# Performance work log

Hardware: AMD Instinct MI355X
Metric: run time of the kernel (lower is better)

## Reference

```python
import jax, jax.numpy as jnp
import numpy as np

T, D = 4096, 2048
H, DK, DV = 6, 256, 512        # heads, head_k_dim, head_v_dim (expand_v=2)
KD, VD = H * DK, H * DV        # 1536, 3072
KSZ = 4                        # conv_size
GEN = D // 8                   # generator reduction 8 -> 256
EPS = 1e-5                     # norm_eps


def setup_inputs() -> dict:
    key = jax.random.key(0)
    ks = jax.random.split(key, 12)
    std = 0.02
    p = lambda i, shape: jax.random.normal(ks[i], shape, jnp.float32) * std
    rng = np.random.default_rng(0)
    A = rng.uniform(0.0, 16.0, H).astype(np.float32)
    dt = np.exp(rng.uniform(0, 1, H) * (np.log(0.1) - np.log(0.001)) + np.log(0.001)).astype(np.float32)
    dt = np.clip(dt, 1e-4, None)
    inv_dt = (dt + np.log(-np.expm1(-dt))).astype(np.float32)
    return {
        'hidden_states': jax.random.normal(ks[0], (T, D), jnp.float32),
        'Wq': p(1, (D, KD)), 'Wk': p(2, (D, KD)), 'Wv': p(3, (D, VD)),
        'Wb': p(4, (D, H)), 'Wa': p(5, (D, H)), 'Wg': p(6, (D, VD)), 'Wo': p(7, (VD, D)),
        'A_log': jnp.asarray(np.log(A)), 'dt_bias': jnp.asarray(inv_dt),
        'conv_w': p(8, (VD, KSZ)), 'gen_w1': p(9, (D, GEN)), 'gen_w2': p(10, (GEN, KSZ)),
        'norm_w': jnp.ones((DV,), jnp.float32),
    }


def _l2norm(x):
    return x * jax.lax.rsqrt(jnp.sum(x * x, -1, keepdims=True) + 1e-6)


def reference(hidden_states, Wq, Wk, Wv, Wb, Wa, Wg, Wo, A_log, dt_bias, conv_w, gen_w1, gen_w2, norm_w):
    h = hidden_states[None]                             # [1,T,D]
    q = jax.nn.silu(h @ Wq)                             # [1,T,KD]
    k = jax.nn.silu(h @ Wk)
    x = h @ Wv                                          # [1,T,VD]
    # dynamic short convolution: per-token kernel added to static depthwise kernel
    dyn = jax.nn.silu(h @ gen_w1) @ gen_w2              # [1,T,KSZ]
    xpad = jnp.pad(x, ((0, 0), (KSZ - 1, 0), (0, 0)))   # causal padding
    v = jnp.zeros_like(x)
    for j in range(KSZ):
        v = v + (conv_w[None, None, :, j] + dyn[:, :, None, j]) * xpad[:, j:j + x.shape[1], :]
    v = jax.nn.silu(v)

    B = 1
    q = _l2norm(q.reshape(B, -1, H, DK))                # use_qk_l2norm_in_kernel=True
    k = _l2norm(k.reshape(B, -1, H, DK))
    v = v.reshape(B, -1, H, DV)
    beta = jax.nn.sigmoid(h @ Wb)                       # [1,T,H]
    g = -jnp.exp(A_log) * jax.nn.softplus(h @ Wa + dt_bias)  # [1,T,H] decay log-gates
    scale = DK ** -0.5

    def step(S, inp):                                   # gated delta rule recurrence
        qt, kt, vt, gt, bt = inp
        S = S * jnp.exp(gt)[..., None, None]            # [B,H,DK,DV]
        dv = (vt - jnp.einsum('bhk,bhkv->bhv', kt, S)) * bt[..., None]
        S = S + kt[..., :, None] * dv[..., None, :]
        ot = jnp.einsum('bhk,bhkv->bhv', qt, S) * scale
        return S, ot

    S0 = jnp.zeros((B, H, DK, DV), jnp.float32)
    tm = lambda a: jnp.moveaxis(a, 1, 0)                # time-major for scan
    _, o = jax.lax.scan(step, S0, (tm(q), tm(k), tm(v), tm(g), tm(beta)))
    o = jnp.moveaxis(o, 0, 1)                           # [1,T,H,DV]

    gate = (h @ Wg).reshape(B, -1, H, DV)
    rms = jax.lax.rsqrt(jnp.mean(o * o, -1, keepdims=True) + EPS)
    o = o * rms * norm_w * jax.nn.silu(gate)            # gated RMSNorm
    o = o.reshape(B, -1, VD) @ Wo                       # [1,T,D]
    return o[0]
```

## Files before the change

### kernel.cpp

```cpp
#include <hip/hip_runtime.h>
#include <hip/hip_bf16.h>
#include <math.h>

#define T_LEN 4096
#define DIM   2048
#define NH    6
#define DK    256
#define DVh   512
#define KD    1536
#define VD    3072
#define CK    64
#define NCHK  (T_LEN / CK)

typedef __attribute__((ext_vector_type(8))) short bf16x8;
typedef __attribute__((ext_vector_type(4))) float f32x4;

__device__ __forceinline__ float silu_f(float v){ return v / (1.f + __expf(-v)); }

__device__ __forceinline__ unsigned short f2bf(float f) {
  unsigned int u = __float_as_uint(f);
  unsigned int r = u + 0x7FFFu + ((u >> 16) & 1u);
  return (unsigned short)(r >> 16);
}
__device__ __forceinline__ float bf2f(unsigned short s) {
  return __uint_as_float(((unsigned int)s) << 16);
}

__global__ __launch_bounds__(256) void cast_bf16(
    const float* __restrict__ in, unsigned short* __restrict__ out)
{
  int i = blockIdx.x * 256 + threadIdx.x;
  float4 v4 = ((const float4*)in)[i];
  ushort4 o4;
  o4.x = f2bf(v4.x); o4.y = f2bf(v4.y); o4.z = f2bf(v4.z); o4.w = f2bf(v4.w);
  ((ushort4*)out)[i] = o4;
}

__global__ __launch_bounds__(256) void tcast(
    const float* __restrict__ in, unsigned short* __restrict__ out, int R, int Cn)
{
  __shared__ float tile[32][33];
  int bx = blockIdx.x * 32;
  int by = blockIdx.y * 32;
  int tx = threadIdx.x & 31, ty = threadIdx.x >> 5;
#pragma unroll
  for (int i = 0; i < 32; i += 8)
    tile[ty + i][tx] = in[(size_t)(by + ty + i) * Cn + bx + tx];
  __syncthreads();
#pragma unroll
  for (int i = 0; i < 32; i += 8)
    out[(size_t)(bx + ty + i) * R + by + tx] = f2bf(tile[tx][ty + i]);
}

__global__ __launch_bounds__(256) void gemm_bt_bf16(
    const unsigned short* __restrict__ A, const unsigned short* __restrict__ BT,
    void* __restrict__ Cout, int M, int N, int K, int act)
{
  __shared__ unsigned short As[128 * 32];
  __shared__ unsigned short Bs[128 * 32];
  const int tid = threadIdx.x;
  const int bm = blockIdx.y * 128, bn = blockIdx.x * 128;
  const int lane = tid & 63, wave = tid >> 6;
  const int wm = (wave >> 1) * 64, wn = (wave & 1) * 64;
  const int fr = lane & 15, kq = lane >> 4;

  f32x4 acc[4][4];
#pragma unroll
  for (int i = 0; i < 4; ++i)
#pragma unroll
    for (int j = 0; j < 4; ++j) acc[i][j] = (f32x4){0.f, 0.f, 0.f, 0.f};

  const int r0 = tid >> 2, c0 = (tid & 3) * 8;
  const int r1 = r0 + 64;

  for (int k0 = 0; k0 < K; k0 += 32) {
    __builtin_amdgcn_global_load_lds(
        (const __attribute__((address_space(1))) unsigned int*)(A + (size_t)(bm + r0) * K + k0 + c0),
        (__attribute__((address_space(3))) unsigned int*)(As + r0 * 32 + c0), 16, 0, 0);
    __builtin_amdgcn_global_load_lds(
        (const __attribute__((address_space(1))) unsigned int*)(A + (size_t)(bm + r1) * K + k0 + c0),
        (__attribute__((address_space(3))) unsigned int*)(As + r1 * 32 + c0), 16, 0, 0);
    __builtin_amdgcn_global_load_lds(
        (const __attribute__((address_space(1))) unsigned int*)(BT + (size_t)(bn + r0) * K + k0 + c0),
        (__attribute__((address_space(3))) unsigned int*)(Bs + r0 * 32 + c0), 16, 0, 0);
    __builtin_amdgcn_global_load_lds(
        (const __attribute__((address_space(1))) unsigned int*)(BT + (size_t)(bn + r1) * K + k0 + c0),
        (__attribute__((address_space(3))) unsigned int*)(Bs + r1 * 32 + c0), 16, 0, 0);
    __syncthreads();

    bf16x8 af[4], bfr[4];
#pragma unroll
    for (int i = 0; i < 4; ++i)
      af[i] = *(const bf16x8*)(As + (wm + i * 16 + fr) * 32 + kq * 8);
#pragma unroll
    for (int j = 0; j < 4; ++j)
      bfr[j] = *(const bf16x8*)(Bs + (wn + j * 16 + fr) * 32 + kq * 8);
#pragma unroll
    for (int i = 0; i < 4; ++i)
#pragma unroll
      for (int j = 0; j < 4; ++j)
        acc[i][j] = __builtin_amdgcn_mfma_f32_16x16x32_bf16(af[i], bfr[j], acc[i][j], 0, 0, 0);
    __syncthreads();
  }

  if (act == 2) {
    unsigned short* C = (unsigned short*)Cout;
#pragma unroll
    for (int i = 0; i < 4; ++i) {
      int rbase = bm + wm + i * 16 + kq * 4;
#pragma unroll
      for (int r = 0; r < 4; ++r) {
        size_t rowoff = (size_t)(rbase + r) * N + bn + wn + fr;
#pragma unroll
        for (int j = 0; j < 4; ++j) C[rowoff + j * 16] = f2bf(acc[i][j][r]);
      }
    }
  } else {
    float* C = (float*)Cout;
#pragma unroll
    for (int i = 0; i < 4; ++i) {
      int rbase = bm + wm + i * 16 + kq * 4;
#pragma unroll
      for (int r = 0; r < 4; ++r) {
        size_t rowoff = (size_t)(rbase + r) * N + bn + wn + fr;
#pragma unroll
        for (int j = 0; j < 4; ++j) {
          float v = acc[i][j][r];
          if (act == 1) v = silu_f(v);
          C[rowoff + j * 16] = v;
        }
      }
    }
  }
}

__global__ __launch_bounds__(256) void proj_dyn(
    const float* __restrict__ tg, const float* __restrict__ w2, float* __restrict__ dyn)
{
  int t = blockIdx.x, tid = threadIdx.x;
  float g = tg[(size_t)t * 256 + tid];
  float p[4];
#pragma unroll
  for (int j = 0; j < 4; ++j) p[j] = g * w2[tid * 4 + j];
#pragma unroll
  for (int j = 0; j < 4; ++j)
    for (int m = 32; m >= 1; m >>= 1) p[j] += __shfl_xor(p[j], m);
  __shared__ float red[4][4];
  if ((tid & 63) == 0) {
    int w = tid >> 6;
#pragma unroll
    for (int j = 0; j < 4; ++j) red[w][j] = p[j];
  }
  __syncthreads();
  if (tid < 4) dyn[(size_t)t * 4 + tid] = red[0][tid] + red[1][tid] + red[2][tid] + red[3][tid];
}

__global__ __launch_bounds__(256) void proj_bg(
    const float* __restrict__ h, const float* __restrict__ Wb, const float* __restrict__ Wa,
    const float* __restrict__ A_log, const float* __restrict__ dt_bias,
    float* __restrict__ beta, float* __restrict__ gout)
{
  int t = blockIdx.x, tid = threadIdx.x;
  float pb[6], pa[6];
#pragma unroll
  for (int j = 0; j < 6; ++j) { pb[j] = 0.f; pa[j] = 0.f; }
  for (int d = tid; d < DIM; d += 256) {
    float hv = h[(size_t)t * DIM + d];
#pragma unroll
    for (int j = 0; j < 6; ++j) {
      pb[j] += hv * Wb[d * 6 + j];
      pa[j] += hv * Wa[d * 6 + j];
    }
  }
#pragma unroll
  for (int j = 0; j < 6; ++j)
    for (int m = 32; m >= 1; m >>= 1) { pb[j] += __shfl_xor(pb[j], m); pa[j] += __shfl_xor(pa[j], m); }
  __shared__ float rb[4][6], ra[4][6];
  if ((tid & 63) == 0) {
    int w = tid >> 6;
#pragma unroll
    for (int j = 0; j < 6; ++j) { rb[w][j] = pb[j]; ra[w][j] = pa[j]; }
  }
  __syncthreads();
  if (tid < 6) {
    int j = tid;
    float sb = rb[0][j] + rb[1][j] + rb[2][j] + rb[3][j];
    float sa = ra[0][j] + ra[1][j] + ra[2][j] + ra[3][j];
    beta[(size_t)t * 6 + j] = 1.f / (1.f + expf(-sb));
    float z = sa + dt_bias[j];
    float sp = (z > 20.f) ? z : log1pf(expf(z));
    gout[(size_t)t * 6 + j] = -expf(A_log[j]) * sp;
  }
}

__global__ __launch_bounds__(256) void conv_kernel(
    const float* __restrict__ x, const float* __restrict__ dyn,
    const float* __restrict__ cw, float* __restrict__ v)
{
  int c = blockIdx.x * 256 + threadIdx.x;
  int t = blockIdx.y;
  float4 w4 = ((const float4*)cw)[c];
  float d0 = dyn[t * 4 + 0], d1 = dyn[t * 4 + 1], d2 = dyn[t * 4 + 2], d3 = dyn[t * 4 + 3];
  float acc = (w4.w + d3) * x[(size_t)t * VD + c];
  if (t >= 1) acc += (w4.z + d2) * x[(size_t)(t - 1) * VD + c];
  if (t >= 2) acc += (w4.y + d1) * x[(size_t)(t - 2) * VD + c];
  if (t >= 3) acc += (w4.x + d0) * x[(size_t)(t - 3) * VD + c];
  v[(size_t)t * VD + c] = silu_f(acc);
}

__global__ __launch_bounds__(64) void l2norm_qk(
    float* __restrict__ q, float* __restrict__ k)
{
  size_t base = (size_t)blockIdx.x * 256;
  int tid = threadIdx.x;
  float4 qv = ((float4*)(q + base))[tid];
  float4 kv = ((float4*)(k + base))[tid];
  float sq = qv.x*qv.x + qv.y*qv.y + qv.z*qv.z + qv.w*qv.w;
  float sk = kv.x*kv.x + kv.y*kv.y + kv.z*kv.z + kv.w*kv.w;
  for (int m = 32; m >= 1; m >>= 1) { sq += __shfl_xor(sq, m); sk += __shfl_xor(sk, m); }
  float rq = rsqrtf(sq + 1e-6f) * 0.0625f;
  float rk = rsqrtf(sk + 1e-6f);
  qv.x *= rq; qv.y *= rq; qv.z *= rq; qv.w *= rq;
  kv.x *= rk; kv.y *= rk; kv.z *= rk; kv.w *= rk;
  ((float4*)(q + base))[tid] = qv;
  ((float4*)(k + base))[tid] = kv;
}

__global__ __launch_bounds__(64) void cumsum_g(
    const float* __restrict__ g, float* __restrict__ c, float* __restrict__ gammas)
{
  int ch = blockIdx.x, h = blockIdx.y;
  int t0 = ch * CK;
  int lane = threadIdx.x;
  float cum = g[(size_t)(t0 + lane) * 6 + h];
  for (int off = 1; off < 64; off <<= 1) {
    float n = __shfl_up(cum, off);
    if (lane >= off) cum += n;
  }
  c[(size_t)h * T_LEN + t0 + lane] = cum;
  if (lane == 63) gammas[h * NCHK + ch] = __expf(cum);
}

__global__ __launch_bounds__(384) void scale_kq(
    const float* __restrict__ q, const float* __restrict__ k, const float* __restrict__ c,
    unsigned short* __restrict__ Qb, unsigned short* __restrict__ Kb)
{
  int t = blockIdx.x;
  int tid = threadIdx.x;
  int h = tid >> 6;
  float w1 = __expf(c[(size_t)h * T_LEN + t]);
  size_t off = (size_t)t * KD + tid * 4;
  float4 qv = *(const float4*)(q + off);
  float4 kv = *(const float4*)(k + off);
  ushort4 qo, ko;
  qo.x = f2bf(w1 * qv.x); qo.y = f2bf(w1 * qv.y); qo.z = f2bf(w1 * qv.z); qo.w = f2bf(w1 * qv.w);
  ko.x = f2bf(w1 * kv.x); ko.y = f2bf(w1 * kv.y); ko.z = f2bf(w1 * kv.z); ko.w = f2bf(w1 * kv.w);
  *(ushort4*)(Qb + off) = qo;
  *(ushort4*)(Kb + off) = ko;
}

__global__ __launch_bounds__(256) void make_khT(
    const float* __restrict__ k, const float* __restrict__ c,
    unsigned short* __restrict__ KhT)
{
  int ch = blockIdx.x, h = blockIdx.y;
  int t0 = ch * CK;
  int tt = threadIdx.x & 63, ks = threadIdx.x >> 6;
  float cend = c[(size_t)h * T_LEN + t0 + 63];
  float w2 = __expf(cend - c[(size_t)h * T_LEN + t0 + tt]);
  size_t obase = ((size_t)(h * NCHK + ch)) * DK * CK;
#pragma unroll 8
  for (int kb2 = 0; kb2 < 64; ++kb2) {
    int kk = ks * 64 + kb2;
    float kv = k[(size_t)(t0 + tt) * KD + h * 256 + kk];
    KhT[obase + (size_t)kk * CK + tt] = f2bf(w2 * kv);
  }
}

__global__ __launch_bounds__(256) void chunk_lp(
    const float* __restrict__ q, const float* __restrict__ k,
    const float* __restrict__ c, const float* __restrict__ beta,
    float* __restrict__ Lg, unsigned short* __restrict__ Pm)
{
  const int ch = blockIdx.x, h = blockIdx.y;
  const int t0 = ch * CK;
  const int tid = threadIdx.x;
  const int w = tid >> 6, lane = tid & 63, fr = lane & 15, kq = lane >> 4;
  __shared__ unsigned short kb[64][264];
  __shared__ unsigned short qb[64][264];
  __shared__ float cs[64], bs[64];
#pragma unroll
  for (int i = 0; i < 16; ++i) {
    int fi = tid + i * 256;
    int r = fi >> 6, d4 = fi & 63;
    float4 kv = *(const float4*)(k + (size_t)(t0 + r) * KD + h * 256 + d4 * 4);
    float4 qv = *(const float4*)(q + (size_t)(t0 + r) * KD + h * 256 + d4 * 4);
    ushort4 k4, q4;
    k4.x = f2bf(kv.x); k4.y = f2bf(kv.y); k4.z = f2bf(kv.z); k4.w = f2bf(kv.w);
    q4.x = f2bf(qv.x); q4.y = f2bf(qv.y); q4.z = f2bf(qv.z); q4.w = f2bf(qv.w);
    *(ushort4*)&kb[r][d4 * 4] = k4;
    *(ushort4*)&qb[r][d4 * 4] = q4;
  }
  if (tid < 64) {
    cs[tid] = c[(size_t)h * T_LEN + t0 + tid];
    bs[tid] = beta[(size_t)(t0 + tid) * 6 + h];
  }
  __syncthreads();

  f32x4 akk[4], aqk[4];
#pragma unroll
  for (int j = 0; j < 4; ++j) { akk[j] = (f32x4){0,0,0,0}; aqk[j] = (f32x4){0,0,0,0}; }
#pragma unroll
  for (int kt = 0; kt < 8; ++kt) {
    bf16x8 ak = *(const bf16x8*)&kb[16 * w + fr][kt * 32 + kq * 8];
    bf16x8 aq = *(const bf16x8*)&qb[16 * w + fr][kt * 32 + kq * 8];
#pragma unroll
    for (int j = 0; j < 4; ++j) {
      bf16x8 b = *(const bf16x8*)&kb[j * 16 + fr][kt * 32 + kq * 8];
      akk[j] = __builtin_amdgcn_mfma_f32_16x16x32_bf16(ak, b, akk[j], 0, 0, 0);
      aqk[j] = __builtin_amdgcn_mfma_f32_16x16x32_bf16(aq, b, aqk[j], 0, 0, 0);
    }
  }
  size_t base = ((size_t)(h * NCHK + ch)) * CK * CK;
#pragma unroll
  for (int j = 0; j < 4; ++j) {
#pragma unroll
    for (int r = 0; r < 4; ++r) {
      int t = 16 * w + kq * 4 + r, col = j * 16 + fr;
      float e = __expf(fminf(cs[t] - cs[col], 0.f));
      Lg[base + t * 64 + col] = (col < t) ? bs[t] * e * akk[j][r] : 0.f;
      Pm[base + t * 64 + col] = f2bf((col <= t) ? e * aqk[j][r] : 0.f);
    }
  }
}

__global__ __launch_bounds__(64) void tri_inv(
    const float* __restrict__ Lg, const float* __restrict__ beta,
    unsigned short* __restrict__ Tm)
{
  const int ch = blockIdx.x, h = blockIdx.y;
  const size_t base = ((size_t)(h * NCHK + ch)) * CK * CK;
  const int j = threadIdx.x;
  __shared__ float Ll[64][65];
  __shared__ float Tl[64][65];
  for (int t = 0; t < 64; ++t) Ll[t][j] = Lg[base + t * 64 + j];
  __syncthreads();
  for (int t = 0; t < 64; ++t) {
    float s;
    if (j > t) s = 0.f;
    else if (j == t) s = 1.f;
    else {
      s = 0.f;
      for (int m = j; m < t; ++m) s -= Ll[t][m] * Tl[m][j];
    }
    Tl[t][j] = s;
  }
  float bj = beta[(size_t)(ch * 64 + j) * 6 + h];
  for (int t = 0; t < 64; ++t) Tm[base + t * 64 + j] = f2bf(Tl[t][j] * bj);
}

__global__ __launch_bounds__(256) void scan_chunk(
    const unsigned short* __restrict__ Kb,
    const unsigned short* __restrict__ Qb,
    const unsigned short* __restrict__ KhT,
    const unsigned short* __restrict__ Tm,
    const unsigned short* __restrict__ Pm,
    const float* __restrict__ gammas,
    float* __restrict__ VO)
{
  const int h = blockIdx.y, sl = blockIdx.x;
  const int tid = threadIdx.x;
  const int w = tid >> 6, lane = tid & 63;
  const int fr = lane & 15, kq = lane >> 4;

  __shared__ unsigned short S0h[16][264];
  __shared__ unsigned short S0l[16][264];
  __shared__ unsigned short XT[16][72];
  __shared__ unsigned short DVT[16][72];

  f32x4 st[4];
#pragma unroll
  for (int i = 0; i < 4; ++i) st[i] = (f32x4){0.f, 0.f, 0.f, 0.f};

  const int colg = h * DVh + sl * 16 + fr;
  const size_t hc0 = (size_t)h * NCHK;

  for (int ch = 0; ch < NCHK; ++ch) {
    const int t0 = ch * CK;
    const size_t cb = hc0 + ch;

    bf16x8 kf[8], qf[8];
    {
      const unsigned short* krow = Kb + (size_t)(t0 + 16 * w + fr) * KD + h * 256 + kq * 8;
      const unsigned short* qrow = Qb + (size_t)(t0 + 16 * w + fr) * KD + h * 256 + kq * 8;
#pragma unroll
      for (int kt = 0; kt < 8; ++kt) {
        kf[kt] = *(const bf16x8*)(krow + kt * 32);
        qf[kt] = *(const bf16x8*)(qrow + kt * 32);
      }
    }
    bf16x8 tf[2], pf[2];
    {
      const unsigned short* trow = Tm + (cb * CK + 16 * w + fr) * CK + kq * 8;
      const unsigned short* prow = Pm + (cb * CK + 16 * w + fr) * CK + kq * 8;
      tf[0] = *(const bf16x8*)(trow); tf[1] = *(const bf16x8*)(trow + 32);
      pf[0] = *(const bf16x8*)(prow); pf[1] = *(const bf16x8*)(prow + 32);
    }
    bf16x8 hf[4][2];
#pragma unroll
    for (int i = 0; i < 4; ++i) {
      const unsigned short* hrow = KhT + (cb * DK + 64 * w + 16 * i + fr) * CK + kq * 8;
      hf[i][0] = *(const bf16x8*)(hrow); hf[i][1] = *(const bf16x8*)(hrow + 32);
    }
    float vld[4];
#pragma unroll
    for (int r = 0; r < 4; ++r)
      vld[r] = VO[(size_t)(t0 + 16 * w + kq * 4 + r) * VD + colg];
    const float gam = gammas[hc0 + ch];

#pragma unroll
    for (int i = 0; i < 4; ++i) {
      ushort4 hi4, lo4;
      {
        float s0 = st[i][0], s1 = st[i][1], s2 = st[i][2], s3 = st[i][3];
        hi4.x = f2bf(s0); lo4.x = f2bf(s0 - bf2f(hi4.x));
        hi4.y = f2bf(s1); lo4.y = f2bf(s1 - bf2f(hi4.y));
        hi4.z = f2bf(s2); lo4.z = f2bf(s2 - bf2f(hi4.z));
        hi4.w = f2bf(s3); lo4.w = f2bf(s3 - bf2f(hi4.w));
      }
      *(ushort4*)&S0h[fr][64 * w + 16 * i + kq * 4] = hi4;
      *(ushort4*)&S0l[fr][64 * w + 16 * i + kq * 4] = lo4;
    }
    __syncthreads();

    {
      f32x4 y = (f32x4){0.f, 0.f, 0.f, 0.f};
#pragma unroll
      for (int kt = 0; kt < 8; ++kt) {
        bf16x8 bh_ = *(const bf16x8*)&S0h[fr][kt * 32 + kq * 8];
        bf16x8 bl_ = *(const bf16x8*)&S0l[fr][kt * 32 + kq * 8];
        y = __builtin_amdgcn_mfma_f32_16x16x32_bf16(kf[kt], bh_, y, 0, 0, 0);
        y = __builtin_amdgcn_mfma_f32_16x16x32_bf16(kf[kt], bl_, y, 0, 0, 0);
      }
      ushort4 x4;
      x4.x = f2bf(vld[0] - y[0]); x4.y = f2bf(vld[1] - y[1]);
      x4.z = f2bf(vld[2] - y[2]); x4.w = f2bf(vld[3] - y[3]);
      *(ushort4*)&XT[fr][16 * w + kq * 4] = x4;
    }
    __syncthreads();

    {
      f32x4 d = (f32x4){0.f, 0.f, 0.f, 0.f};
#pragma unroll
      for (int kt = 0; kt < 2; ++kt) {
        bf16x8 b = *(const bf16x8*)&XT[fr][kt * 32 + kq * 8];
        d = __builtin_amdgcn_mfma_f32_16x16x32_bf16(tf[kt], b, d, 0, 0, 0);
      }
      ushort4 d4;
      d4.x = f2bf(d[0]); d4.y = f2bf(d[1]); d4.z = f2bf(d[2]); d4.w = f2bf(d[3]);
      *(ushort4*)&DVT[fr][16 * w + kq * 4] = d4;
    }
    __syncthreads();

    {
      f32x4 o = (f32x4){0.f, 0.f, 0.f, 0.f};
#pragma unroll
      for (int kt = 0; kt < 8; ++kt) {
        bf16x8 bh_ = *(const bf16x8*)&S0h[fr][kt * 32 + kq * 8];
        bf16x8 bl_ = *(const bf16x8*)&S0l[fr][kt * 32 + kq * 8];
        o = __builtin_amdgcn_mfma_f32_16x16x32_bf16(qf[kt], bh_, o, 0, 0, 0);
        o = __builtin_amdgcn_mfma_f32_16x16x32_bf16(qf[kt], bl_, o, 0, 0, 0);
      }
#pragma unroll
      for (int kt = 0; kt < 2; ++kt) {
        bf16x8 b = *(const bf16x8*)&DVT[fr][kt * 32 + kq * 8];
        o = __builtin_amdgcn_mfma_f32_16x16x32_bf16(pf[kt], b, o, 0, 0, 0);
      }
#pragma unroll
      for (int r = 0; r < 4; ++r)
        VO[(size_t)(t0 + 16 * w + kq * 4 + r) * VD + colg] = o[r];
    }

#pragma unroll
    for (int i = 0; i < 4; ++i) {
      st[i][0] *= gam; st[i][1] *= gam; st[i][2] *= gam; st[i][3] *= gam;
#pragma unroll
      for (int kt = 0; kt < 2; ++kt) {
        bf16x8 b = *(const bf16x8*)&DVT[fr][kt * 32 + kq * 8];
        st[i] = __builtin_amdgcn_mfma_f32_16x16x32_bf16(hf[i][kt], b, st[i], 0, 0, 0);
      }
    }
    __syncthreads();
  }
}

__global__ __launch_bounds__(256) void norm_gate(
    const float* __restrict__ o, const unsigned short* __restrict__ gate,
    const float* __restrict__ nw, unsigned short* __restrict__ out)
{
  int th = blockIdx.x, tid = threadIdx.x;
  size_t base = (size_t)th * DVh;
  float x0 = o[base + tid], x1 = o[base + 256 + tid];
  float ss = x0 * x0 + x1 * x1;
  for (int m = 32; m >= 1; m >>= 1) ss += __shfl_xor(ss, m);
  __shared__ float red[4];
  if ((tid & 63) == 0) red[tid >> 6] = ss;
  __syncthreads();
  float rms = rsqrtf((red[0] + red[1] + red[2] + red[3]) * (1.f / 512.f) + 1e-5f);
  float g0 = bf2f(gate[base + tid]), g1 = bf2f(gate[base + 256 + tid]);
  out[base + tid]       = f2bf(x0 * rms * nw[tid]       * silu_f(g0));
  out[base + 256 + tid] = f2bf(x1 * rms * nw[tid + 256] * silu_f(g1));
}

extern "C" void kernel_launch(void* const* d_in, const int* in_sizes, int n_in,
                              void* d_out, int out_size, void* d_ws, size_t ws_size,
                              hipStream_t stream)
{
  const float* h       = (const float*)d_in[0];
  const float* Wq      = (const float*)d_in[1];
  const float* Wk      = (const float*)d_in[2];
  const float* Wv      = (const float*)d_in[3];
  const float* Wb      = (const float*)d_in[4];
  const float* Wa      = (const float*)d_in[5];
  const float* Wg      = (const float*)d_in[6];
  const float* Wo      = (const float*)d_in[7];
  const float* A_log   = (const float*)d_in[8];
  const float* dt_bias = (const float*)d_in[9];
  const float* conv_w  = (const float*)d_in[10];
  const float* gen_w1  = (const float*)d_in[11];
  const float* gen_w2  = (const float*)d_in[12];
  const float* norm_w  = (const float*)d_in[13];
  float* out = (float*)d_out;

  const size_t TK = (size_t)T_LEN * KD, TV = (size_t)T_LEN * VD, TD = (size_t)T_LEN * DIM;

  float* ws   = (float*)d_ws;
  float* q    = ws;
  float* k    = q    + TK;
  float* x    = k    + TK;
  float* v    = x    + TV;
  float* tg   = v    + TV;
  float* dyn  = tg   + (size_t)T_LEN * 256;
  float* beta = dyn  + (size_t)T_LEN * 4;
  float* g    = beta + (size_t)T_LEN * 6;
  float* c    = g    + (size_t)T_LEN * 6;
  float* gam  = c    + (size_t)NH * T_LEN;
  float* fend = gam  + 512;
  unsigned short* bh      = (unsigned short*)fend;
  unsigned short* wT      = bh      + TD;
  unsigned short* gate_bf = wT      + (size_t)DIM * VD;
  unsigned short* go_bf   = gate_bf + TV;
  unsigned short* Kb_s  = bh;
  unsigned short* Qb_s  = (unsigned short*)x;
  unsigned short* KhT_s = Qb_s + TK;
  unsigned short* Tm_s  = KhT_s + TK;
  unsigned short* Pm_s  = Tm_s + (size_t)NH * NCHK * CK * CK;
  float* Lg = (float*)go_bf;

  dim3 blk(256);
  cast_bf16<<<(TD / 4) / 256, blk, 0, stream>>>(h, bh);
  tcast<<<dim3(KD / 32, DIM / 32), blk, 0, stream>>>(Wq, wT, DIM, KD);
  gemm_bt_bf16<<<dim3(KD / 128, T_LEN / 128), blk, 0, stream>>>(bh, wT, q, T_LEN, KD, DIM, 1);
  tcast<<<dim3(KD / 32, DIM / 32), blk, 0, stream>>>(Wk, wT, DIM, KD);
  gemm_bt_bf16<<<dim3(KD / 128, T_LEN / 128), blk, 0, stream>>>(bh, wT, k, T_LEN, KD, DIM, 1);
  tcast<<<dim3(VD / 32, DIM / 32), blk, 0, stream>>>(Wv, wT, DIM, VD);
  gemm_bt_bf16<<<dim3(VD / 128, T_LEN / 128), blk, 0, stream>>>(bh, wT, x, T_LEN, VD, DIM, 0);
  tcast<<<dim3(VD / 32, DIM / 32), blk, 0, stream>>>(Wg, wT, DIM, VD);
  gemm_bt_bf16<<<dim3(VD / 128, T_LEN / 128), blk, 0, stream>>>(bh, wT, gate_bf, T_LEN, VD, DIM, 2);
  tcast<<<dim3(256 / 32, DIM / 32), blk, 0, stream>>>(gen_w1, wT, DIM, 256);
  gemm_bt_bf16<<<dim3(256 / 128, T_LEN / 128), blk, 0, stream>>>(bh, wT, tg, T_LEN, 256, DIM, 1);

  proj_dyn<<<T_LEN, blk, 0, stream>>>(tg, gen_w2, dyn);
  proj_bg<<<T_LEN, blk, 0, stream>>>(h, Wb, Wa, A_log, dt_bias, beta, g);
  conv_kernel<<<dim3(VD / 256, T_LEN), blk, 0, stream>>>(x, dyn, conv_w, v);
  l2norm_qk<<<T_LEN * NH, 64, 0, stream>>>(q, k);

  cumsum_g<<<dim3(NCHK, NH), 64, 0, stream>>>(g, c, gam);
  scale_kq<<<T_LEN, 384, 0, stream>>>(q, k, c, Qb_s, Kb_s);
  make_khT<<<dim3(NCHK, NH), blk, 0, stream>>>(k, c, KhT_s);
  chunk_lp<<<dim3(NCHK, NH), blk, 0, stream>>>(q, k, c, beta, Lg, Pm_s);
  tri_inv<<<dim3(NCHK, NH), 64, 0, stream>>>(Lg, beta, Tm_s);

  scan_chunk<<<dim3(DVh / 16, NH), blk, 0, stream>>>(Kb_s, Qb_s, KhT_s, Tm_s, Pm_s, gam, v);

  norm_gate<<<T_LEN * NH, blk, 0, stream>>>(v, gate_bf, norm_w, go_bf);
  tcast<<<dim3(DIM / 32, VD / 32), blk, 0, stream>>>(Wo, wT, VD, DIM);
  gemm_bt_bf16<<<dim3(DIM / 128, T_LEN / 128), blk, 0, stream>>>(go_bf, wT, out, T_LEN, DIM, VD, 0);
}
```

Before: 1.071 ms.

## Prefetch next-chunk K and V in the recurrence loop with LDS-only barriers

The chunked delta-rule recurrence kernel now loads the next chunk's K fragments and V values during the current chunk, using ping-pong register buffers and a loop unrolled by two. Barriers become s_waitcnt lgkmcnt(0) plus s_barrier wrapped in sched_barrier, so they no longer wait on outstanding global loads. The hi/lo MFMA chains are split into independent accumulators to cut dependent-MFMA latency. In exchange, register pressure rises, which may lower occupancy, and float summation order changes slightly.

```diff
diff --git a/kernel.cpp b/kernel.cpp
--- a/kernel.cpp
+++ b/kernel.cpp
@@ -24,6 +24,13 @@
 }
 __device__ __forceinline__ float bf2f(unsigned short s) {
   return __uint_as_float(((unsigned int)s) << 16);
+}
+
+__device__ __forceinline__ void bar_lds() {
+  __builtin_amdgcn_sched_barrier(0);
+  asm volatile("s_waitcnt lgkmcnt(0)" ::: "memory");
+  __builtin_amdgcn_s_barrier();
+  __builtin_amdgcn_sched_barrier(0);
 }
 
 __global__ __launch_bounds__(256) void cast_bf16(
@@ -385,113 +392,109 @@
   const int colg = h * DVh + sl * 16 + fr;
   const size_t hc0 = (size_t)h * NCHK;
 
-  for (int ch = 0; ch < NCHK; ++ch) {
-    const int t0 = ch * CK;
-    const size_t cb = hc0 + ch;
-
-    bf16x8 kf[8], qf[8];
-    {
-      const unsigned short* krow = Kb + (size_t)(t0 + 16 * w + fr) * KD + h * 256 + kq * 8;
-      const unsigned short* qrow = Qb + (size_t)(t0 + 16 * w + fr) * KD + h * 256 + kq * 8;
-#pragma unroll
-      for (int kt = 0; kt < 8; ++kt) {
-        kf[kt] = *(const bf16x8*)(krow + kt * 32);
-        qf[kt] = *(const bf16x8*)(qrow + kt * 32);
-      }
-    }
-    bf16x8 tf[2], pf[2];
-    {
-      const unsigned short* trow = Tm + (cb * CK + 16 * w + fr) * CK + kq * 8;
-      const unsigned short* prow = Pm + (cb * CK + 16 * w + fr) * CK + kq * 8;
-      tf[0] = *(const bf16x8*)(trow); tf[1] = *(const bf16x8*)(trow + 32);
-      pf[0] = *(const bf16x8*)(prow); pf[1] = *(const bf16x8*)(prow + 32);
-    }
-    bf16x8 hf[4][2];
-#pragma unroll
-    for (int i = 0; i < 4; ++i) {
-      const unsigned short* hrow = KhT + (cb * DK + 64 * w + 16 * i + fr) * CK + kq * 8;
-      hf[i][0] = *(const bf16x8*)(hrow); hf[i][1] = *(const bf16x8*)(hrow + 32);
-    }
-    float vld[4];
-#pragma unroll
-    for (int r = 0; r < 4; ++r)
-      vld[r] = VO[(size_t)(t0 + 16 * w + kq * 4 + r) * VD + colg];
-    const float gam = gammas[hc0 + ch];
-
-#pragma unroll
-    for (int i = 0; i < 4; ++i) {
-      ushort4 hi4, lo4;
-      {
-        float s0 = st[i][0], s1 = st[i][1], s2 = st[i][2], s3 = st[i][3];
-        hi4.x = f2bf(s0); lo4.x = f2bf(s0 - bf2f(hi4.x));
-        hi4.y = f2bf(s1); lo4.y = f2bf(s1 - bf2f(hi4.y));
-        hi4.z = f2bf(s2); lo4.z = f2bf(s2 - bf2f(hi4.z));
-        hi4.w = f2bf(s3); lo4.w = f2bf(s3 - bf2f(hi4.w));
-      }
-      *(ushort4*)&S0h[fr][64 * w + 16 * i + kq * 4] = hi4;
-      *(ushort4*)&S0l[fr][64 * w + 16 * i + kq * 4] = lo4;
-    }
-    __syncthreads();
-
-    {
-      f32x4 y = (f32x4){0.f, 0.f, 0.f, 0.f};
-#pragma unroll
-      for (int kt = 0; kt < 8; ++kt) {
-        bf16x8 bh_ = *(const bf16x8*)&S0h[fr][kt * 32 + kq * 8];
-        bf16x8 bl_ = *(const bf16x8*)&S0l[fr][kt * 32 + kq * 8];
-        y = __builtin_amdgcn_mfma_f32_16x16x32_bf16(kf[kt], bh_, y, 0, 0, 0);
-        y = __builtin_amdgcn_mfma_f32_16x16x32_bf16(kf[kt], bl_, y, 0, 0, 0);
-      }
-      ushort4 x4;
-      x4.x = f2bf(vld[0] - y[0]); x4.y = f2bf(vld[1] - y[1]);
-      x4.z = f2bf(vld[2] - y[2]); x4.w = f2bf(vld[3] - y[3]);
-      *(ushort4*)&XT[fr][16 * w + kq * 4] = x4;
-    }
-    __syncthreads();
-
-    {
-      f32x4 d = (f32x4){0.f, 0.f, 0.f, 0.f};
-#pragma unroll
-      for (int kt = 0; kt < 2; ++kt) {
-        bf16x8 b = *(const bf16x8*)&XT[fr][kt * 32 + kq * 8];
-        d = __builtin_amdgcn_mfma_f32_16x16x32_bf16(tf[kt], b, d, 0, 0, 0);
-      }
-      ushort4 d4;
-      d4.x = f2bf(d[0]); d4.y = f2bf(d[1]); d4.z = f2bf(d[2]); d4.w = f2bf(d[3]);
-      *(ushort4*)&DVT[fr][16 * w + kq * 4] = d4;
-    }
-    __syncthreads();
-
-    {
-      f32x4 o = (f32x4){0.f, 0.f, 0.f, 0.f};
-#pragma unroll
-      for (int kt = 0; kt < 8; ++kt) {
-        bf16x8 bh_ = *(const bf16x8*)&S0h[fr][kt * 32 + kq * 8];
-        bf16x8 bl_ = *(const bf16x8*)&S0l[fr][kt * 32 + kq * 8];
-        o = __builtin_amdgcn_mfma_f32_16x16x32_bf16(qf[kt], bh_, o, 0, 0, 0);
-        o = __builtin_amdgcn_mfma_f32_16x16x32_bf16(qf[kt], bl_, o, 0, 0, 0);
-      }
-#pragma unroll
-      for (int kt = 0; kt < 2; ++kt) {
-        bf16x8 b = *(const bf16x8*)&DVT[fr][kt * 32 + kq * 8];
-        o = __builtin_amdgcn_mfma_f32_16x16x32_bf16(pf[kt], b, o, 0, 0, 0);
-      }
-#pragma unroll
-      for (int r = 0; r < 4; ++r)
-        VO[(size_t)(t0 + 16 * w + kq * 4 + r) * VD + colg] = o[r];
-    }
-
-#pragma unroll
-    for (int i = 0; i < 4; ++i) {
-      st[i][0] *= gam; st[i][1] *= gam; st[i][2] *= gam; st[i][3] *= gam;
-#pragma unroll
-      for (int kt = 0; kt < 2; ++kt) {
-        bf16x8 b = *(const bf16x8*)&DVT[fr][kt * 32 + kq * 8];
-        st[i] = __builtin_amdgcn_mfma_f32_16x16x32_bf16(hf[i][kt], b, st[i], 0, 0, 0);
-      }
-    }
-    __syncthreads();
-  }
+  bf16x8 kfA[8], kfB[8];
+  float vlA[4], vlB[4];
+
+#define PREF_KV(KF, VL, chn) do { \
+    const unsigned short* krow_ = Kb + (size_t)((chn) * CK + 16 * w + fr) * KD + h * 256 + kq * 8; \
+    _Pragma("unroll") \
+    for (int kt = 0; kt < 8; ++kt) KF[kt] = *(const bf16x8*)(krow_ + kt * 32); \
+    _Pragma("unroll") \
+    for (int r = 0; r < 4; ++r) VL[r] = VO[(size_t)((chn) * CK + 16 * w + kq * 4 + r) * VD + colg]; \
+  } while (0)
+
+#define CHUNK_BODY(chx, KF, VL, KFN, VLN) do { \
+    const int ch_ = (chx); \
+    const int t0_ = ch_ * CK; \
+    const size_t cb_ = hc0 + ch_; \
+     \
+    bf16x8 qf[8]; \
+    { const unsigned short* qrow_ = Qb + (size_t)(t0_ + 16 * w + fr) * KD + h * 256 + kq * 8; \
+      _Pragma("unroll") \
+      for (int kt = 0; kt < 8; ++kt) qf[kt] = *(const bf16x8*)(qrow_ + kt * 32); } \
+    bf16x8 tf[2], pf[2]; \
+    { const unsigned short* trow_ = Tm + (cb_ * CK + 16 * w + fr) * CK + kq * 8; \
+      const unsigned short* prow_ = Pm + (cb_ * CK + 16 * w + fr) * CK + kq * 8; \
+      tf[0] = *(const bf16x8*)(trow_); tf[1] = *(const bf16x8*)(trow_ + 32); \
+      pf[0] = *(const bf16x8*)(prow_); pf[1] = *(const bf16x8*)(prow_ + 32); } \
+    bf16x8 hfr[4][2]; \
+    _Pragma("unroll") \
+    for (int i = 0; i < 4; ++i) { \
+      const unsigned short* hrow_ = KhT + (cb_ * DK + 64 * w + 16 * i + fr) * CK + kq * 8; \
+      hfr[i][0] = *(const bf16x8*)(hrow_); hfr[i][1] = *(const bf16x8*)(hrow_ + 32); } \
+    const float gam_ = gammas[cb_]; \
+     \
+    _Pragma("unroll") \
+    for (int i = 0; i < 4; ++i) { \
+      ushort4 hi4, lo4; \
+      float s0 = st[i][0], s1 = st[i][1], s2 = st[i][2], s3 = st[i][3]; \
+      hi4.x = f2bf(s0); lo4.x = f2bf(s0 - bf2f(hi4.x)); \
+      hi4.y = f2bf(s1); lo4.y = f2bf(s1 - bf2f(hi4.y)); \
+      hi4.z = f2bf(s2); lo4.z = f2bf(s2 - bf2f(hi4.z)); \
+      hi4.w = f2bf(s3); lo4.w = f2bf(s3 - bf2f(hi4.w)); \
+      *(ushort4*)&S0h[fr][64 * w + 16 * i + kq * 4] = hi4; \
+      *(ushort4*)&S0l[fr][64 * w + 16 * i + kq * 4] = lo4; } \
+     \
+    { const int chn_ = (ch_ + 1 < NCHK) ? ch_ + 1 : ch_; PREF_KV(KFN, VLN, chn_); } \
+    bar_lds(); \
+     \
+    { f32x4 yh = (f32x4){0.f,0.f,0.f,0.f}, yl = (f32x4){0.f,0.f,0.f,0.f}; \
+      _Pragma("unroll") \
+      for (int kt = 0; kt < 8; ++kt) { \
+        bf16x8 bh_ = *(const bf16x8*)&S0h[fr][kt * 32 + kq * 8]; \
+        bf16x8 bl_ = *(const bf16x8*)&S0l[fr][kt * 32 + kq * 8]; \
+        yh = __builtin_amdgcn_mfma_f32_16x16x32_bf16(KF[kt], bh_, yh, 0, 0, 0); \
+        yl = __builtin_amdgcn_mfma_f32_16x16x32_bf16(KF[kt], bl_, yl, 0, 0, 0); } \
+      ushort4 x4; \
+      x4.x = f2bf(VL[0] - (yh[0] + yl[0])); \
+      x4.y = f2bf(VL[1] - (yh[1] + yl[1])); \
+      x4.z = f2bf(VL[2] - (yh[2] + yl[2])); \
+      x4.w = f2bf(VL[3] - (yh[3] + yl[3])); \
+      *(ushort4*)&XT[fr][16 * w + kq * 4] = x4; } \
+    bar_lds(); \
+     \
+    { f32x4 d = (f32x4){0.f,0.f,0.f,0.f}; \
+      _Pragma("unroll") \
+      for (int kt = 0; kt < 2; ++kt) { \
+        bf16x8 b_ = *(const bf16x8*)&XT[fr][kt * 32 + kq * 8]; \
+        d = __builtin_amdgcn_mfma_f32_16x16x32_bf16(tf[kt], b_, d, 0, 0, 0); } \
+      ushort4 d4; \
+      d4.x = f2bf(d[0]); d4.y = f2bf(d[1]); d4.z = f2bf(d[2]); d4.w = f2bf(d[3]); \
+      *(ushort4*)&DVT[fr][16 * w + kq * 4] = d4; } \
+    bar_lds(); \
+     \
+    { f32x4 oh = (f32x4){0.f,0.f,0.f,0.f}, ol = (f32x4){0.f,0.f,0.f,0.f}, op = (f32x4){0.f,0.f,0.f,0.f}; \
+      _Pragma("unroll") \
+      for (int kt = 0; kt < 8; ++kt) { \
+        bf16x8 bh_ = *(const bf16x8*)&S0h[fr][kt * 32 + kq * 8]; \
+        bf16x8 bl_ = *(const bf16x8*)&S0l[fr][kt * 32 + kq * 8]; \
+        oh = __builtin_amdgcn_mfma_f32_16x16x32_bf16(qf[kt], bh_, oh, 0, 0, 0); \
+        ol = __builtin_amdgcn_mfma_f32_16x16x32_bf16(qf[kt], bl_, ol, 0, 0, 0); } \
+      _Pragma("unroll") \
+      for (int kt = 0; kt < 2; ++kt) { \
+        bf16x8 b_ = *(const bf16x8*)&DVT[fr][kt * 32 + kq * 8]; \
+        op = __builtin_amdgcn_mfma_f32_16x16x32_bf16(pf[kt], b_, op, 0, 0, 0); } \
+      _Pragma("unroll") \
+      for (int r = 0; r < 4; ++r) \
+        VO[(size_t)(t0_ + 16 * w + kq * 4 + r) * VD + colg] = oh[r] + ol[r] + op[r]; } \
+     \
+    _Pragma("unroll") \
+    for (int i = 0; i < 4; ++i) { \
+      st[i][0] *= gam_; st[i][1] *= gam_; st[i][2] *= gam_; st[i][3] *= gam_; \
+      _Pragma("unroll") \
+      for (int kt = 0; kt < 2; ++kt) { \
+        bf16x8 b_ = *(const bf16x8*)&DVT[fr][kt * 32 + kq * 8]; \
+        st[i] = __builtin_amdgcn_mfma_f32_16x16x32_bf16(hfr[i][kt], b_, st[i], 0, 0, 0); } } \
+    bar_lds(); \
+  } while (0)
+
+  PREF_KV(kfA, vlA, 0);
+  for (int ch = 0; ch < NCHK; ch += 2) {
+    CHUNK_BODY(ch,     kfA, vlA, kfB, vlB);
+    CHUNK_BODY(ch + 1, kfB, vlB, kfA, vlA);
+  }
+#undef CHUNK_BODY
+#undef PREF_KV
 }
 
 __global__ __launch_bounds__(256) void norm_gate(
```

Result: no change. 1.074 ms (+0.3%).
